# Kernel tuning notes

Hardware: AMD Instinct MI355X
Metric: run time of the kernel (lower is better)

## Reference

```python
import jax, jax.numpy as jnp
import numpy as np

B, S, D, H = 64, 512, 1024, 1024

def setup_inputs() -> dict:
    key = jax.random.key(0)
    k1, k2, k3 = jax.random.split(key, 3)
    inp = jax.random.normal(k1, (B, S, D), dtype=jnp.float32)
    # gate order: i, f, o, c_hat ; Wx ~ fc1.weight (no bias), Wh ~ fc2.weight, b ~ fc2.bias
    Wx = jax.random.normal(k2, (4, H, D), dtype=jnp.float32) * 0.02
    Wh = jax.random.normal(k3, (4, H, H), dtype=jnp.float32) * 0.02
    b = jnp.zeros((4, H), dtype=jnp.float32)
    return {"input": inp, "Wx": Wx, "Wh": Wh, "b": b}

def reference(input, Wx, Wh, b):
    # Precompute all input projections for all 4 gates in one big GEMM:
    # (S, B, 4, H) with time leading for scan
    x_proj = jnp.einsum('bsd,ghd->sbgh', input, Wx)

    def step(carry, xp):
        h, c = carry
        # hidden projections for all 4 gates: one batched GEMM per step
        g = xp + jnp.einsum('bh,gkh->bgk', h, Wh) + b  # (B, 4, H)
        i_t = jax.nn.sigmoid(g[:, 0])
        f_t = jax.nn.sigmoid(g[:, 1])
        o_t = jax.nn.sigmoid(g[:, 2])
        c_hat = jnp.tanh(g[:, 3])
        c_new = f_t * c + i_t * c_hat
        h_new = o_t * jnp.tanh(c_new)
        return (h_new, c_new), h_new

    h0 = jnp.zeros((input.shape[0], Wh.shape[-1]), dtype=input.dtype)
    c0 = jnp.zeros_like(h0)
    (h_last, c_last), ys = jax.lax.scan(step, (h0, c0), x_proj)
    output = jnp.transpose(ys, (1, 0, 2))  # (B, S, H)
    return output, (h_last, c_last)
```

## Files before the change

### kernel.cpp

```cpp
#include <hip/hip_runtime.h>

#define B_ 64
#define S_ 512
#define D_ 1024
#define H_ 1024
#define NBLK 256
#define NT 512
#define TB 8
#define NSLOT 4

typedef __bf16 v8bf __attribute__((ext_vector_type(8)));
typedef float v4f __attribute__((ext_vector_type(4)));
typedef float f32x4 __attribute__((ext_vector_type(4)));
typedef unsigned long long u64;
typedef unsigned u32;

#define MFMA __builtin_amdgcn_mfma_f32_16x16x32_bf16

__device__ inline v8bf cvt8(const float* p) {
  f32x4 a = *(const f32x4*)p;
  f32x4 b = *(const f32x4*)(p + 4);
  v8bf r;
  r[0] = (__bf16)a[0]; r[1] = (__bf16)a[1]; r[2] = (__bf16)a[2]; r[3] = (__bf16)a[3];
  r[4] = (__bf16)b[0]; r[5] = (__bf16)b[1]; r[6] = (__bf16)b[2]; r[7] = (__bf16)b[3];
  return r;
}

__global__ __launch_bounds__(NT, 2)
void lstm_persist(const float* __restrict__ x,
                  const float* __restrict__ Wx,
                  const float* __restrict__ Wh,
                  const float* __restrict__ bias,
                  float* __restrict__ out,
                  __bf16* __restrict__ hblk,
                  u32* __restrict__ flags)
{
  extern __shared__ char smem[];
  v8bf* wlds = (v8bf*)smem;
  v4f*  xacc = (v4f*)(smem + 65536);
  u32*  seq  = (u32*)(smem + 65536 + 16384);

  const int tid  = threadIdx.x;
  const int nb   = blockIdx.x;
  const int w8   = tid >> 6;
  const int l    = tid & 63;
  const int lm   = l & 15;
  const int quad = l >> 4;
  const int sw   = lm & 7;

  for (int i = tid; i < 16 * 256; i += NT) {
    const int nl  = i >> 8;
    const int kc  = i & 255;
    const int g   = nl >> 2;
    const int col = (nb << 2) + (nl & 3);
    const int k   = kc << 3;
    const float* src = (k < D_)
        ? (Wx + ((size_t)(g * H_ + col) * D_ + k))
        : (Wh + ((size_t)(g * H_ + col) * H_ + (k - D_)));
    wlds[(nl << 8) + (kc ^ (nl & 7))] = cvt8(src);
  }
  if (tid < 128) seq[tid] = 0;

  __syncthreads();

  u32* xseq = seq;
  u32* hseq = seq + 64;

  if (w8 < 4) {
    const int w   = w8;
    const int myb = (w << 4) + lm;
    for (int t = 0; t < S_; ++t) {
      if (t >= NSLOT) {
        while (__hip_atomic_load(&hseq[w << 4], __ATOMIC_ACQUIRE,
                                 __HIP_MEMORY_SCOPE_WORKGROUP)
               < (u32)(t - NSLOT + 1)) {
          __builtin_amdgcn_s_sleep(1);
        }
      }
      v4f a0 = {0.f,0.f,0.f,0.f}, a1 = {0.f,0.f,0.f,0.f};
      const float* xrow = x + ((size_t)(myb * S_ + t)) * D_ + (quad << 3);
      #pragma unroll 4
      for (int cc = 0; cc < 16; ++cc) {
        const int c0 = cc * 2, c1 = cc * 2 + 1;
        v8bf f0 = cvt8(xrow + (c0 << 5));
        a0 = MFMA(f0, wlds[(lm << 8) + (((c0 << 2) + quad) ^ sw)], a0, 0, 0, 0);
        v8bf f1 = cvt8(xrow + (c1 << 5));
        a1 = MFMA(f1, wlds[(lm << 8) + (((c1 << 2) + quad) ^ sw)], a1, 0, 0, 0);
      }
      xacc[((t & (NSLOT - 1)) << 8) + (w << 6) + l] = a0 + a1;
      asm volatile("s_waitcnt lgkmcnt(0)" ::: "memory");
      if (l == 0)
        __hip_atomic_store(&xseq[w << 4], (u32)(t + 1), __ATOMIC_RELEASE,
                           __HIP_MEMORY_SCOPE_WORKGROUP);
    }
  } else {
    const int s     = w8 & 3;
    const int myb   = (s << 4) + lm;
    const int myb4  = myb << 2;
    const int mycol = (nb << 2) + quad;
    float bv[4];
    #pragma unroll
    for (int g = 0; g < 4; ++g) bv[g] = bias[g * H_ + mycol];

    float c_reg = 0.f;
    float obuf[TB];

    const u32* fw     = flags + (s << 8);
    u32*       myflag = flags + (s << 8) + nb;

    for (int t = 0; t < S_; ++t) {
      while (__hip_atomic_load(&xseq[s << 4], __ATOMIC_ACQUIRE,
                               __HIP_MEMORY_SCOPE_WORKGROUP) < (u32)(t + 1)) {
        __builtin_amdgcn_s_sleep(1);
      }
      const v4f xa = xacc[((t & (NSLOT - 1)) << 8) + (s << 6) + l];
      asm volatile("s_waitcnt lgkmcnt(0)" ::: "memory");
      if (l == 0)
        __hip_atomic_store(&hseq[s << 4], (u32)(t + 1), __ATOMIC_RELEASE,
                           __HIP_MEMORY_SCOPE_WORKGROUP);

      v4f acc0 = xa, acc1 = {0.f,0.f,0.f,0.f};

      if (t > 0) {
        const u32 tu = (u32)t;
        for (;;) {
          const u32 f0 = __hip_atomic_load(fw + (l << 2) + 0,
              __ATOMIC_RELAXED, __HIP_MEMORY_SCOPE_AGENT);
          const u32 f1 = __hip_atomic_load(fw + (l << 2) + 1,
              __ATOMIC_RELAXED, __HIP_MEMORY_SCOPE_AGENT);
          const u32 f2 = __hip_atomic_load(fw + (l << 2) + 2,
              __ATOMIC_RELAXED, __HIP_MEMORY_SCOPE_AGENT);
          const u32 f3 = __hip_atomic_load(fw + (l << 2) + 3,
              __ATOMIC_RELAXED, __HIP_MEMORY_SCOPE_AGENT);
          if (__all((f0 >= tu) & (f1 >= tu) & (f2 >= tu) & (f3 >= tu))) break;
          __builtin_amdgcn_s_sleep(1);
        }
        asm volatile("" ::: "memory");

        const __bf16* hb = hblk + ((t & 1) ? (1 << 16) : 0);
        #pragma unroll 4
        for (int cc = 0; cc < 16; ++cc) {
          const int c0 = cc * 2, c1 = cc * 2 + 1;
          const int j0 = (quad << 1) + (c0 << 3);
          const int j1 = (quad << 1) + (c1 << 3);
          union { u64 q[2]; v8bf v; } h0, h1;
          h0.q[0] = __hip_atomic_load((const u64*)(hb + (j0 << 8) + myb4),
              __ATOMIC_RELAXED, __HIP_MEMORY_SCOPE_AGENT);
          h0.q[1] = __hip_atomic_load((const u64*)(hb + ((j0 + 1) << 8) + myb4),
              __ATOMIC_RELAXED, __HIP_MEMORY_SCOPE_AGENT);
          h1.q[0] = __hip_atomic_load((const u64*)(hb + (j1 << 8) + myb4),
              __ATOMIC_RELAXED, __HIP_MEMORY_SCOPE_AGENT);
          h1.q[1] = __hip_atomic_load((const u64*)(hb + ((j1 + 1) << 8) + myb4),
              __ATOMIC_RELAXED, __HIP_MEMORY_SCOPE_AGENT);
          acc0 = MFMA(h0.v, wlds[(lm << 8) + ((128 + (c0 << 2) + quad) ^ sw)], acc0, 0, 0, 0);
          acc1 = MFMA(h1.v, wlds[(lm << 8) + ((128 + (c1 << 2) + quad) ^ sw)], acc1, 0, 0, 0);
        }
      }

      v4f accs = acc0 + acc1;

      float gv[4];
      const int rsel = lm & 3;
      #pragma unroll
      for (int g = 0; g < 4; ++g) {
        const int srcl = ((lm >> 2) << 4) + (g << 2) + quad;
        float t0 = __shfl(accs[0], srcl, 64);
        float t1 = __shfl(accs[1], srcl, 64);
        float t2 = __shfl(accs[2], srcl, 64);
        float t3 = __shfl(accs[3], srcl, 64);
        gv[g] = (rsel == 0 ? t0 : rsel == 1 ? t1 : rsel == 2 ? t2 : t3) + bv[g];
      }

      const float it = 1.f / (1.f + __expf(-gv[0]));
      const float ft = 1.f / (1.f + __expf(-gv[1]));
      const float ot = 1.f / (1.f + __expf(-gv[2]));
      const float ch = 1.f - 2.f / (__expf(2.f * gv[3]) + 1.f);
      c_reg = ft * c_reg + it * ch;
      const float hn = ot * (1.f - 2.f / (__expf(2.f * c_reg) + 1.f));

      {
        union { __bf16 b; unsigned short u; } hb2;
        hb2.b = (__bf16)hn;
        __hip_atomic_store(
            (unsigned short*)(hblk + (((t + 1) & 1) ? (1 << 16) : 0)
                              + (nb << 8) + myb4 + quad),
            hb2.u, __ATOMIC_RELAXED, __HIP_MEMORY_SCOPE_AGENT);
      }

      asm volatile("s_waitcnt vmcnt(0)" ::: "memory");
      __hip_atomic_store(myflag, (u32)(t + 1), __ATOMIC_RELAXED,
                         __HIP_MEMORY_SCOPE_AGENT);

      obuf[t & (TB - 1)] = hn;
      if ((t & (TB - 1)) == TB - 1) {
        #pragma unroll
        for (int i = 0; i < TB; ++i)
          __builtin_nontemporal_store(
              obuf[i], &out[((size_t)(myb * S_ + (t - TB + 1 + i))) * H_ + mycol]);
      }
      if (t == S_ - 1) {
        __builtin_nontemporal_store(
            hn, &out[(size_t)B_ * S_ * H_ + (size_t)myb * H_ + mycol]);
        __builtin_nontemporal_store(
            c_reg, &out[(size_t)B_ * S_ * H_ + (size_t)(B_ * H_)
                        + (size_t)myb * H_ + mycol]);
      }
    }
  }
}

extern "C" void kernel_launch(void* const* d_in, const int* in_sizes, int n_in,
                              void* d_out, int out_size, void* d_ws, size_t ws_size,
                              hipStream_t stream) {
  const float* x    = (const float*)d_in[0];
  const float* Wx   = (const float*)d_in[1];
  const float* Wh   = (const float*)d_in[2];
  const float* bias = (const float*)d_in[3];
  float* out = (float*)d_out;

  u32*    flags = (u32*)d_ws;
  __bf16* hblk  = (__bf16*)((char*)d_ws + 4096);

  hipMemsetAsync(d_ws, 0, 4096, stream);

  const size_t lds_bytes = 65536 + NSLOT * 4 * 64 * 16 + 512;
  lstm_persist<<<dim3(NBLK), dim3(NT), lds_bytes, stream>>>(
      x, Wx, Wh, bias, out, hblk, flags);
}
```

Before: 6.731 ms.

## Embed step tags in hidden-state words to drop separate flag polling

Measured after the change: 7.529 ms. 1.12x slower.

```diff
diff --git a/kernel.cpp b/kernel.cpp
--- a/kernel.cpp
+++ b/kernel.cpp
@@ -12,8 +12,9 @@
 typedef __bf16 v8bf __attribute__((ext_vector_type(8)));
 typedef float v4f __attribute__((ext_vector_type(4)));
 typedef float f32x4 __attribute__((ext_vector_type(4)));
+typedef unsigned uint32;
 typedef unsigned long long u64;
-typedef unsigned u32;
+typedef unsigned uint32x4 __attribute__((ext_vector_type(4)));
 
 #define MFMA __builtin_amdgcn_mfma_f32_16x16x32_bf16
 
@@ -32,13 +33,12 @@
                   const float* __restrict__ Wh,
                   const float* __restrict__ bias,
                   float* __restrict__ out,
-                  __bf16* __restrict__ hblk,
-                  u32* __restrict__ flags)
+                  uint32* __restrict__ hblk)
 {
   extern __shared__ char smem[];
-  v8bf* wlds = (v8bf*)smem;
-  v4f*  xacc = (v4f*)(smem + 65536);
-  u32*  seq  = (u32*)(smem + 65536 + 16384);
+  v8bf*   wlds = (v8bf*)smem;
+  v4f*    xacc = (v4f*)(smem + 65536);
+  uint32* seq  = (uint32*)(smem + 65536 + 16384);
 
   const int tid  = threadIdx.x;
   const int nb   = blockIdx.x;
@@ -63,8 +63,8 @@
 
   __syncthreads();
 
-  u32* xseq = seq;
-  u32* hseq = seq + 64;
+  uint32* xseq = seq;
+  uint32* hseq = seq + 64;
 
   if (w8 < 4) {
     const int w   = w8;
@@ -73,7 +73,7 @@
       if (t >= NSLOT) {
         while (__hip_atomic_load(&hseq[w << 4], __ATOMIC_ACQUIRE,
                                  __HIP_MEMORY_SCOPE_WORKGROUP)
-               < (u32)(t - NSLOT + 1)) {
+               < (uint32)(t - NSLOT + 1)) {
           __builtin_amdgcn_s_sleep(1);
         }
       }
@@ -90,13 +90,12 @@
       xacc[((t & (NSLOT - 1)) << 8) + (w << 6) + l] = a0 + a1;
       asm volatile("s_waitcnt lgkmcnt(0)" ::: "memory");
       if (l == 0)
-        __hip_atomic_store(&xseq[w << 4], (u32)(t + 1), __ATOMIC_RELEASE,
+        __hip_atomic_store(&xseq[w << 4], (uint32)(t + 1), __ATOMIC_RELEASE,
                            __HIP_MEMORY_SCOPE_WORKGROUP);
     }
   } else {
     const int s     = w8 & 3;
     const int myb   = (s << 4) + lm;
-    const int myb4  = myb << 2;
     const int mycol = (nb << 2) + quad;
     float bv[4];
     #pragma unroll
@@ -104,57 +103,87 @@
 
     float c_reg = 0.f;
     float obuf[TB];
-
-    const u32* fw     = flags + (s << 8);
-    u32*       myflag = flags + (s << 8) + nb;
+    v4f acc0, acc1;
+
+#define ISSUE_GRP(Rn, g)                                                      \
+  {                                                                           \
+    const char* gb = hbase + ((g) << 16);                                     \
+    _Pragma("unroll")                                                         \
+    for (int cc = 0; cc < 8; ++cc) {                                          \
+      u64 a_ = (u64)(uintptr_t)(gb + (cc << 13));                             \
+      asm volatile("global_load_dwordx4 %0, %2, off sc1\n\t"                  \
+                   "global_load_dwordx4 %1, %2, off offset:1024 sc1"          \
+                   : "=&v"(Rn[2 * cc]), "=&v"(Rn[2 * cc + 1])                 \
+                   : "v"(a_) : "memory");                                     \
+    }                                                                         \
+  }
+
+#define CHECK_CONSUME(Rn, g)                                                  \
+  {                                                                           \
+    for (;;) {                                                                \
+      int ok = 1;                                                             \
+      _Pragma("unroll")                                                       \
+      for (int i = 0; i < 16; ++i) {                                          \
+        ok &= ((Rn[i][0] & 0xFFFFu) == tu);                                   \
+        ok &= ((Rn[i][1] & 0xFFFFu) == tu);                                   \
+        ok &= ((Rn[i][2] & 0xFFFFu) == tu);                                   \
+        ok &= ((Rn[i][3] & 0xFFFFu) == tu);                                   \
+      }                                                                       \
+      if (__all(ok)) break;                                                   \
+      __builtin_amdgcn_s_sleep(1);                                            \
+      ISSUE_GRP(Rn, g);                                                       \
+      asm volatile("s_waitcnt vmcnt(0)" ::: "memory");                        \
+      __builtin_amdgcn_sched_barrier(0);                                      \
+    }                                                                         \
+    _Pragma("unroll")                                                         \
+    for (int cc = 0; cc < 8; ++cc) {                                          \
+      const int c_ = (g) * 8 + cc;                                            \
+      union { uint32 u[4]; v8bf v; } A_;                                      \
+      A_.u[0] = __builtin_amdgcn_perm(Rn[2 * cc][1], Rn[2 * cc][0], 0x07060302u); \
+      A_.u[1] = __builtin_amdgcn_perm(Rn[2 * cc][3], Rn[2 * cc][2], 0x07060302u); \
+      A_.u[2] = __builtin_amdgcn_perm(Rn[2 * cc + 1][1], Rn[2 * cc + 1][0], 0x07060302u); \
+      A_.u[3] = __builtin_amdgcn_perm(Rn[2 * cc + 1][3], Rn[2 * cc + 1][2], 0x07060302u); \
+      v8bf bf_ = wlds[(lm << 8) + ((128 + (c_ << 2) + quad) ^ sw)];           \
+      if (cc & 1) acc1 = MFMA(A_.v, bf_, acc1, 0, 0, 0);                      \
+      else        acc0 = MFMA(A_.v, bf_, acc0, 0, 0, 0);                      \
+    }                                                                         \
+  }
 
     for (int t = 0; t < S_; ++t) {
       while (__hip_atomic_load(&xseq[s << 4], __ATOMIC_ACQUIRE,
-                               __HIP_MEMORY_SCOPE_WORKGROUP) < (u32)(t + 1)) {
+                               __HIP_MEMORY_SCOPE_WORKGROUP) < (uint32)(t + 1)) {
         __builtin_amdgcn_s_sleep(1);
       }
       const v4f xa = xacc[((t & (NSLOT - 1)) << 8) + (s << 6) + l];
       asm volatile("s_waitcnt lgkmcnt(0)" ::: "memory");
       if (l == 0)
-        __hip_atomic_store(&hseq[s << 4], (u32)(t + 1), __ATOMIC_RELEASE,
+        __hip_atomic_store(&hseq[s << 4], (uint32)(t + 1), __ATOMIC_RELEASE,
                            __HIP_MEMORY_SCOPE_WORKGROUP);
 
-      v4f acc0 = xa, acc1 = {0.f,0.f,0.f,0.f};
+      acc0 = xa;
+      acc1 = (v4f){0.f, 0.f, 0.f, 0.f};
 
       if (t > 0) {
-        const u32 tu = (u32)t;
-        for (;;) {
-          const u32 f0 = __hip_atomic_load(fw + (l << 2) + 0,
-              __ATOMIC_RELAXED, __HIP_MEMORY_SCOPE_AGENT);
-          const u32 f1 = __hip_atomic_load(fw + (l << 2) + 1,
-              __ATOMIC_RELAXED, __HIP_MEMORY_SCOPE_AGENT);
-          const u32 f2 = __hip_atomic_load(fw + (l << 2) + 2,
-              __ATOMIC_RELAXED, __HIP_MEMORY_SCOPE_AGENT);
-          const u32 f3 = __hip_atomic_load(fw + (l << 2) + 3,
-              __ATOMIC_RELAXED, __HIP_MEMORY_SCOPE_AGENT);
-          if (__all((f0 >= tu) & (f1 >= tu) & (f2 >= tu) & (f3 >= tu))) break;
-          __builtin_amdgcn_s_sleep(1);
-        }
-        asm volatile("" ::: "memory");
-
-        const __bf16* hb = hblk + ((t & 1) ? (1 << 16) : 0);
-        #pragma unroll 4
-        for (int cc = 0; cc < 16; ++cc) {
-          const int c0 = cc * 2, c1 = cc * 2 + 1;
-          const int j0 = (quad << 1) + (c0 << 3);
-          const int j1 = (quad << 1) + (c1 << 3);
-          union { u64 q[2]; v8bf v; } h0, h1;
-          h0.q[0] = __hip_atomic_load((const u64*)(hb + (j0 << 8) + myb4),
-              __ATOMIC_RELAXED, __HIP_MEMORY_SCOPE_AGENT);
-          h0.q[1] = __hip_atomic_load((const u64*)(hb + ((j0 + 1) << 8) + myb4),
-              __ATOMIC_RELAXED, __HIP_MEMORY_SCOPE_AGENT);
-          h1.q[0] = __hip_atomic_load((const u64*)(hb + (j1 << 8) + myb4),
-              __ATOMIC_RELAXED, __HIP_MEMORY_SCOPE_AGENT);
-          h1.q[1] = __hip_atomic_load((const u64*)(hb + ((j1 + 1) << 8) + myb4),
-              __ATOMIC_RELAXED, __HIP_MEMORY_SCOPE_AGENT);
-          acc0 = MFMA(h0.v, wlds[(lm << 8) + ((128 + (c0 << 2) + quad) ^ sw)], acc0, 0, 0, 0);
-          acc1 = MFMA(h1.v, wlds[(lm << 8) + ((128 + (c1 << 2) + quad) ^ sw)], acc1, 0, 0, 0);
-        }
+        const uint32 tu = (uint32)t;
+        const char* hbase = (const char*)(hblk + ((t & 1) ? 65536 : 0))
+                            + (quad << 11) + (myb << 4);
+        uint32x4 R0[16], R1[16];
+        ISSUE_GRP(R0, 0);
+        ISSUE_GRP(R1, 1);
+        asm volatile("s_waitcnt vmcnt(16)" ::: "memory");
+        __builtin_amdgcn_sched_barrier(0);
+        CHECK_CONSUME(R0, 0);
+        ISSUE_GRP(R0, 2);
+        asm volatile("s_waitcnt vmcnt(16)" ::: "memory");
+        __builtin_amdgcn_sched_barrier(0);
+        CHECK_CONSUME(R1, 1);
+        ISSUE_GRP(R1, 3);
+        asm volatile("s_waitcnt vmcnt(16)" ::: "memory");
+        __builtin_amdgcn_sched_barrier(0);
+        CHECK_CONSUME(R0, 2);
+        asm volatile("s_waitcnt vmcnt(0)" ::: "memory");
+        __builtin_amdgcn_sched_barrier(0);
+        CHECK_CONSUME(R1, 3);
       }
 
       v4f accs = acc0 + acc1;
@@ -181,15 +210,11 @@
       {
         union { __bf16 b; unsigned short u; } hb2;
         hb2.b = (__bf16)hn;
-        __hip_atomic_store(
-            (unsigned short*)(hblk + (((t + 1) & 1) ? (1 << 16) : 0)
-                              + (nb << 8) + myb4 + quad),
-            hb2.u, __ATOMIC_RELAXED, __HIP_MEMORY_SCOPE_AGENT);
-      }
-
-      asm volatile("s_waitcnt vmcnt(0)" ::: "memory");
-      __hip_atomic_store(myflag, (u32)(t + 1), __ATOMIC_RELAXED,
-                         __HIP_MEMORY_SCOPE_AGENT);
+        const uint32 word = ((uint32)hb2.u << 16) | (uint32)(t + 1);
+        __hip_atomic_store(hblk + (((t + 1) & 1) ? 65536 : 0)
+                           + (nb << 8) + (myb << 2) + quad,
+                           word, __ATOMIC_RELAXED, __HIP_MEMORY_SCOPE_AGENT);
+      }
 
       obuf[t & (TB - 1)] = hn;
       if ((t & (TB - 1)) == TB - 1) {
@@ -206,6 +231,8 @@
                         + (size_t)myb * H_ + mycol]);
       }
     }
+#undef ISSUE_GRP
+#undef CHECK_CONSUME
   }
 }
 
@@ -218,12 +245,9 @@
   const float* bias = (const float*)d_in[3];
   float* out = (float*)d_out;
 
-  u32*    flags = (u32*)d_ws;
-  __bf16* hblk  = (__bf16*)((char*)d_ws + 4096);
-
-  hipMemsetAsync(d_ws, 0, 4096, stream);
+  uint32* hblk = (uint32*)d_ws;
 
   const size_t lds_bytes = 65536 + NSLOT * 4 * 64 * 16 + 512;
   lstm_persist<<<dim3(NBLK), dim3(NT), lds_bytes, stream>>>(
-      x, Wx, Wh, bias, out, hblk, flags);
+      x, Wx, Wh, bias, out, hblk);
 }
```
